# Kernel optimization log

Measured on AMD Instinct MI355X. Metric: run time of the kernel, lower is better.

Reference implementation:

```python
import jax, jax.numpy as jnp
import numpy as np

B, D, NTXT, H = 16384, 512, 4096, 1024


def _linear_params(key, fan_in, fan_out):
    kw, kb = jax.random.split(key)
    s = 1.0 / np.sqrt(fan_in)
    W = jax.random.uniform(kw, (fan_in, fan_out), jnp.float32, -s, s)
    b = jax.random.uniform(kb, (fan_out,), jnp.float32, -s, s)
    return W, b


def setup_inputs() -> dict:
    key = jax.random.key(0)
    ks = jax.random.split(key, 9)
    img_features = jax.random.normal(ks[0], (B, D), jnp.float32)
    txt_features = jax.random.normal(ks[1], (D, NTXT), jnp.float32)
    target_ind = jax.random.randint(ks[2], (B,), 0, NTXT, jnp.int32)
    Wi0, bi0 = _linear_params(ks[3], D, H)
    Wi1, bi1 = _linear_params(ks[4], H, H)
    Wi2, bi2 = _linear_params(ks[5], H, D)
    Wt0, bt0 = _linear_params(ks[6], D, H)
    Wt1, bt1 = _linear_params(ks[7], H, H)
    Wt2, bt2 = _linear_params(ks[8], H, D)
    logit_scale = jnp.asarray(np.log(1.0 / 0.07), jnp.float32)
    temp = jnp.asarray(1.0, jnp.float32)
    return {
        "img_features": img_features, "txt_features": txt_features,
        "target_ind": target_ind, "temp": temp,
        "Wi0": Wi0, "bi0": bi0, "Wi1": Wi1, "bi1": bi1, "Wi2": Wi2, "bi2": bi2,
        "Wt0": Wt0, "bt0": bt0, "Wt1": Wt1, "bt1": bt1, "Wt2": Wt2, "bt2": bt2,
        "logit_scale": logit_scale,
    }


def _mlp(x, params):
    # ReLU after every layer except the last (matches MLP.forward)
    for W, b in params[:-1]:
        x = jax.nn.relu(x @ W + b)
    W, b = params[-1]
    return x @ W + b


def reference(img_features, txt_features, target_ind, temp,
              Wi0, bi0, Wi1, bi1, Wi2, bi2,
              Wt0, bt0, Wt1, bt1, Wt2, bt2, logit_scale):
    p_img = _mlp(img_features, [(Wi0, bi0), (Wi1, bi1), (Wi2, bi2)])          # [B, D]
    p_txt = _mlp(txt_features.T, [(Wt0, bt0), (Wt1, bt1), (Wt2, bt2)])        # [N, D]

    sim = (p_img @ p_txt.T) * jnp.exp(logit_scale)                            # [B, N]
    sim = sim / jnp.linalg.norm(sim, axis=-1, keepdims=True)
    out_logits = sim / jnp.linalg.norm(sim, axis=-1, keepdims=True)           # faithful double-normalize

    # vectorized form of the per-sample Python-loop softmax-CE in MLP_CLIP_loss
    logp = jax.nn.log_softmax(out_logits / temp, axis=-1)                     # [B, N]
    picked = jnp.take_along_axis(logp, target_ind[:, None].astype(jnp.int32), axis=1)[:, 0]
    loss = -jnp.mean(picked)

    # accuracy branch (uses unscaled similarity, row-normalized)
    sim_clip = p_img @ p_txt.T
    sim_clip = sim_clip / jnp.linalg.norm(sim_clip, axis=-1, keepdims=True)
    acc = jnp.sum(jnp.argmax(sim_clip, axis=1).astype(jnp.int32) == target_ind)
    return loss, acc
```

## Files before the change

### kernel.cpp

```cpp
#include <hip/hip_runtime.h>
#include <cstdint>
#include <cstddef>

#define B_ROWS 16384
#define D_DIM  512
#define NTXT_N 4096
#define H_DIM  1024

typedef __attribute__((ext_vector_type(8))) short short8;
typedef __attribute__((ext_vector_type(4))) float f32x4;

__device__ __forceinline__ ushort f2bf(float x) {
    union { float f; uint32_t u; } c; c.f = x;
    const uint32_t u = c.u;
    return (ushort)((u + 0x7fffu + ((u >> 16) & 1u)) >> 16);
}
__device__ __forceinline__ float bf2f(ushort h) {
    union { uint32_t u; float f; } c; c.u = ((uint32_t)h) << 16;
    return c.f;
}

#define GLDS16(gp, lp) __builtin_amdgcn_global_load_lds( \
    (const __attribute__((address_space(1))) void*)(gp),  \
    (__attribute__((address_space(3))) void*)(lp), 16, 0, 0)

__device__ __forceinline__ void xcd_remap(int& bx, int& by) {
    const int nx = gridDim.x, ny = gridDim.y;
    const int nwg = nx * ny;
    const int bid = by * nx + bx;
    const int q = nwg >> 3, r = nwg & 7;
    const int xcd = bid & 7, idx = bid >> 3;
    const int nb = (xcd < r ? xcd * (q + 1) : r * (q + 1) + (xcd - r) * q) + idx;
    bx = nb % nx; by = nb / nx;
}

__global__ void init_kernel(int* acc) {
    if (threadIdx.x == 0 && blockIdx.x == 0) *acc = 0;
}

__global__ void tsplit_kernel(const float* __restrict__ in, ushort* __restrict__ oh,
                              ushort* __restrict__ ol, int R, int C, int cbase)
{
    __shared__ float tile[32][33];
    const int c0 = blockIdx.x * 32, r0 = blockIdx.y * 32;
    const int tx = threadIdx.x, ty = threadIdx.y;
    #pragma unroll
    for (int j = 0; j < 32; j += 8)
        tile[ty + j][tx] = in[(size_t)(r0 + ty + j) * C + cbase + c0 + tx];
    __syncthreads();
    #pragma unroll
    for (int j = 0; j < 32; j += 8) {
        const float v = tile[tx][ty + j];
        const ushort h = f2bf(v);
        const size_t idx = (size_t)(c0 + ty + j) * R + r0 + tx;
        oh[idx] = h;
        ol[idx] = f2bf(v - bf2f(h));
    }
}

__global__ void csplit_kernel(const float* __restrict__ in, ushort* __restrict__ oh,
                              ushort* __restrict__ ol, int n)
{
    const int i = (blockIdx.x * 256 + threadIdx.x) * 4;
    if (i >= n) return;
    const float4 f = *(const float4*)&in[i];
    ushort4 h, l;
    h.x = f2bf(f.x); l.x = f2bf(f.x - bf2f(h.x));
    h.y = f2bf(f.y); l.y = f2bf(f.y - bf2f(h.y));
    h.z = f2bf(f.z); l.z = f2bf(f.z - bf2f(h.z));
    h.w = f2bf(f.w); l.w = f2bf(f.w - bf2f(h.w));
    *(ushort4*)&oh[i] = h;
    *(ushort4*)&ol[i] = l;
}

template<int OMODE, bool RELU, bool BIAS>
__global__ __launch_bounds__(256, 2)
void gemm_mfma_kernel(const ushort* __restrict__ Ah, const ushort* __restrict__ Al,
                      const ushort* __restrict__ Bh, const ushort* __restrict__ Bl,
                      const float* __restrict__ bias,
                      float* __restrict__ Cf, ushort* __restrict__ Ch, ushort* __restrict__ Cl,
                      int M, int N, int K)
{
    __shared__ __align__(16) ushort Ahs[128 * 32];
    __shared__ __align__(16) ushort Als[128 * 32];
    __shared__ __align__(16) ushort Bhs[128 * 32];
    __shared__ __align__(16) ushort Bls[128 * 32];

    const int tid  = threadIdx.x;
    const int lane = tid & 63;
    const int w    = tid >> 6;
    const int wr   = w >> 1, wc = w & 1;

    int bxi = blockIdx.x, byi = blockIdx.y;
    xcd_remap(bxi, byi);
    const int bm = byi * 128, bn = bxi * 128;

    const int    srow  = w * 32 + (lane >> 2);
    const int    scol  = (((lane & 3) ^ ((lane >> 3) & 3)) << 3);
    const size_t aoff0 = (size_t)(bm + srow) * K + scol;
    const size_t boff0 = (size_t)(bn + srow) * K + scol;

    f32x4 acc[4][4];
    #pragma unroll
    for (int m = 0; m < 4; ++m)
        #pragma unroll
        for (int n = 0; n < 4; ++n)
            acc[m][n] = (f32x4)0.0f;

    const int frow = lane & 15;
    const int sl   = (frow >> 1) & 3;
    const int kslot = (lane >> 4) ^ sl;
    const int koff  = kslot << 3;

    for (int k0 = 0; k0 < K; k0 += 32) {
        #pragma unroll
        for (int j = 0; j < 2; ++j) {
            const size_t go = (size_t)j * 16 * K + k0;
            const int    lo = w * 1024 + j * 512;
            GLDS16(Ah + aoff0 + go, &Ahs[lo]);
            GLDS16(Al + aoff0 + go, &Als[lo]);
            GLDS16(Bh + boff0 + go, &Bhs[lo]);
            GLDS16(Bl + boff0 + go, &Bls[lo]);
        }
        __syncthreads();

        short8 a_h[4], a_l[4], b_h[4], b_l[4];
        #pragma unroll
        for (int m = 0; m < 4; ++m) {
            const int off = (wr * 64 + m * 16 + frow) * 32 + koff;
            a_h[m] = *(const short8*)&Ahs[off];
            a_l[m] = *(const short8*)&Als[off];
        }
        #pragma unroll
        for (int n = 0; n < 4; ++n) {
            const int off = (wc * 64 + n * 16 + frow) * 32 + koff;
            b_h[n] = *(const short8*)&Bhs[off];
            b_l[n] = *(const short8*)&Bls[off];
        }
        #pragma unroll
        for (int m = 0; m < 4; ++m)
            #pragma unroll
            for (int n = 0; n < 4; ++n) {
                acc[m][n] = __builtin_amdgcn_mfma_f32_16x16x32_bf16(a_h[m], b_h[n], acc[m][n], 0, 0, 0);
                acc[m][n] = __builtin_amdgcn_mfma_f32_16x16x32_bf16(a_h[m], b_l[n], acc[m][n], 0, 0, 0);
                acc[m][n] = __builtin_amdgcn_mfma_f32_16x16x32_bf16(a_l[m], b_h[n], acc[m][n], 0, 0, 0);
            }
        __syncthreads();
    }

    const int crow0 = bm + wr * 64 + (lane >> 4) * 4;
    const int ccol0 = bn + wc * 64 + (lane & 15);
    #pragma unroll
    for (int m = 0; m < 4; ++m)
        #pragma unroll
        for (int n = 0; n < 4; ++n) {
            const int col = ccol0 + n * 16;
            const float bv = BIAS ? bias[col] : 0.0f;
            #pragma unroll
            for (int q = 0; q < 4; ++q) {
                float v = acc[m][n][q] + bv;
                if (RELU) v = fmaxf(v, 0.0f);
                const size_t idx = (size_t)(crow0 + m * 16 + q) * N + col;
                if (OMODE == 0) {
                    Cf[idx] = v;
                } else {
                    const ushort h = f2bf(v);
                    Ch[idx] = h;
                    Cl[idx] = f2bf(v - bf2f(h));
                }
            }
        }
}

__global__ __launch_bounds__(256) void rowreduce_kernel(
    const float* __restrict__ sim, const int* __restrict__ tgt,
    const float* __restrict__ temp_p, float* __restrict__ perrow,
    int* __restrict__ acc_cnt, int row0)
{
    const int row = blockIdx.x;
    const float* srow = sim + (size_t)row * NTXT_N;
    const int tid = threadIdx.x;

    float v[16];
    #pragma unroll
    for (int q = 0; q < 4; ++q) {
        float4 f = *(const float4*)&srow[4 * tid + 1024 * q];
        v[4 * q + 0] = f.x; v[4 * q + 1] = f.y; v[4 * q + 2] = f.z; v[4 * q + 3] = f.w;
    }

    float ss = 0.0f, mx = -3.4e38f; int mi = 0x7fffffff;
    #pragma unroll
    for (int q = 0; q < 4; ++q)
        #pragma unroll
        for (int r = 0; r < 4; ++r) {
            const int j = 4 * tid + 1024 * q + r;
            const float x = v[4 * q + r];
            ss = fmaf(x, x, ss);
            if (x > mx) { mx = x; mi = j; }
            else if (x == mx && j < mi) mi = j;
        }

    #pragma unroll
    for (int off = 32; off; off >>= 1) {
        ss += __shfl_down(ss, off);
        const float omx = __shfl_down(mx, off);
        const int   omi = __shfl_down(mi, off);
        if (omx > mx || (omx == mx && omi < mi)) { mx = omx; mi = omi; }
    }

    __shared__ float sws[4], swm[4];
    __shared__ int   swi[4];
    __shared__ float bC, bMx;
    __shared__ int   bAmax;
    const int w = tid >> 6, lane = tid & 63;
    if (lane == 0) { sws[w] = ss; swm[w] = mx; swi[w] = mi; }
    __syncthreads();
    if (tid == 0) {
        float tss = 0.0f, tmx = -3.4e38f; int tmi = 0x7fffffff;
        #pragma unroll
        for (int i = 0; i < 4; ++i) {
            tss += sws[i];
            if (swm[i] > tmx || (swm[i] == tmx && swi[i] < tmi)) { tmx = swm[i]; tmi = swi[i]; }
        }
        const float inv_nr = 1.0f / sqrtf(tss);
        const float n2 = sqrtf(tss * inv_nr * inv_nr);
        const float Cv = inv_nr / (n2 * temp_p[0]);
        bC = Cv; bMx = tmx * Cv; bAmax = tmi;
    }
    __syncthreads();
    const float Cv = bC, mxx = bMx;

    float es = 0.0f;
    #pragma unroll
    for (int q = 0; q < 16; ++q) es += expf(v[q] * Cv - mxx);
    #pragma unroll
    for (int off = 32; off; off >>= 1) es += __shfl_down(es, off);
    if (lane == 0) sws[w] = es;
    __syncthreads();
    if (tid == 0) {
        const float tes = sws[0] + sws[1] + sws[2] + sws[3];
        const float lse = mxx + logf(tes);
        const int t = tgt[row0 + row];
        perrow[row0 + row] = lse - srow[t] * Cv;
        if (bAmax == t) atomicAdd(acc_cnt, 1);
    }
}

__global__ __launch_bounds__(256) void finalize_kernel(
    const float* __restrict__ perrow, const int* __restrict__ acc_cnt,
    float* __restrict__ out)
{
    __shared__ float red[256];
    const int tid = threadIdx.x;
    float s = 0.0f;
    for (int i = tid; i < B_ROWS; i += 256) s += perrow[i];
    red[tid] = s;
    __syncthreads();
    for (int st = 128; st; st >>= 1) {
        if (tid < st) red[tid] += red[tid + st];
        __syncthreads();
    }
    if (tid == 0) {
        out[0] = red[0] / (float)B_ROWS;
        out[1] = (float)(*acc_cnt);
    }
}

extern "C" void kernel_launch(void* const* d_in, const int* in_sizes, int n_in,
                              void* d_out, int out_size, void* d_ws, size_t ws_size,
                              hipStream_t stream)
{
    const float* img  = (const float*)d_in[0];
    const float* txt  = (const float*)d_in[1];
    const int*   tgt  = (const int*)  d_in[2];
    const float* temp = (const float*)d_in[3];
    const float* Wf[6] = { (const float*)d_in[4],  (const float*)d_in[6],  (const float*)d_in[8],
                           (const float*)d_in[10], (const float*)d_in[12], (const float*)d_in[14] };
    const float* bf[6] = { (const float*)d_in[5],  (const float*)d_in[7],  (const float*)d_in[9],
                           (const float*)d_in[11], (const float*)d_in[13], (const float*)d_in[15] };
    float* out = (float*)d_out;

    const int wK[6] = { D_DIM, H_DIM, H_DIM, D_DIM, H_DIM, H_DIM };
    const int wN[6] = { H_DIM, H_DIM, D_DIM, H_DIM, H_DIM, D_DIM };

    auto need = [&](size_t ch, size_t sc) -> size_t {
        size_t wt = 0;
        for (int i = 0; i < 6; ++i) wt += (size_t)wK[i] * wN[i] * 2 * 2;
        const size_t a01 = 2 * (ch * H_DIM * 2 * 2);
        const size_t pt  = (size_t)NTXT_N * D_DIM * 2 * 2;
        const size_t sim = sc * NTXT_N * 4;
        return wt + a01 + pt + sim + (size_t)B_ROWS * 4 + (size_t)64 * 1024;
    };
    const size_t ladder[][2] = { {16384, 4096}, {16384, 2048}, {8192, 4096}, {8192, 2048},
                                 {4096, 2048},  {4096, 1024},  {2048, 1024}, {1024, 1024} };
    size_t CH = 1024, SIMCH = 512;
    for (auto& e : ladder)
        if (need(e[0], e[1]) <= ws_size) { CH = e[0]; SIMCH = e[1]; break; }

    uint8_t* p = (uint8_t*)d_ws;
    auto alloc = [&](size_t bytes) -> void* {
        void* r = (void*)p; p += (bytes + 255) & ~(size_t)255; return r;
    };
    ushort* WTh[6]; ushort* WTl[6];
    for (int i = 0; i < 6; ++i) {
        WTh[i] = (ushort*)alloc((size_t)wK[i] * wN[i] * 2);
        WTl[i] = (ushort*)alloc((size_t)wK[i] * wN[i] * 2);
    }
    ushort* A0h = (ushort*)alloc(CH * H_DIM * 2);
    ushort* A0l = (ushort*)alloc(CH * H_DIM * 2);
    ushort* A1h = (ushort*)alloc(CH * H_DIM * 2);
    ushort* A1l = (ushort*)alloc(CH * H_DIM * 2);
    ushort* PTh = (ushort*)alloc((size_t)NTXT_N * D_DIM * 2);
    ushort* PTl = (ushort*)alloc((size_t)NTXT_N * D_DIM * 2);
    float*  SIM = (float*)alloc(SIMCH * NTXT_N * 4);
    float*  PERROW = (float*)alloc((size_t)B_ROWS * 4);
    int*    ACC = (int*)alloc(64);
    ushort* XBh = A1h;  ushort* XBl = A1l;
    ushort* PIh = A0h;  ushort* PIl = A0l;

    init_kernel<<<1, 64, 0, stream>>>(ACC);

    for (int i = 0; i < 6; ++i)
        tsplit_kernel<<<dim3(wN[i] / 32, wK[i] / 32), dim3(32, 8), 0, stream>>>(
            Wf[i], WTh[i], WTl[i], wK[i], wN[i], 0);

    const size_t CHT = CH < (size_t)NTXT_N ? CH : (size_t)NTXT_N;
    for (size_t n0 = 0; n0 < NTXT_N; n0 += CHT) {
        tsplit_kernel<<<dim3(CHT / 32, D_DIM / 32), dim3(32, 8), 0, stream>>>(
            txt, XBh, XBl, D_DIM, NTXT_N, (int)n0);
        gemm_mfma_kernel<1, true, true><<<dim3(H_DIM / 128, CHT / 128), 256, 0, stream>>>(
            XBh, XBl, WTh[3], WTl[3], bf[3], nullptr, A0h, A0l, (int)CHT, H_DIM, D_DIM);
        gemm_mfma_kernel<1, true, true><<<dim3(H_DIM / 128, CHT / 128), 256, 0, stream>>>(
            A0h, A0l, WTh[4], WTl[4], bf[4], nullptr, A1h, A1l, (int)CHT, H_DIM, H_DIM);
        gemm_mfma_kernel<1, false, true><<<dim3(D_DIM / 128, CHT / 128), 256, 0, stream>>>(
            A1h, A1l, WTh[5], WTl[5], bf[5], nullptr,
            PTh + n0 * D_DIM, PTl + n0 * D_DIM, (int)CHT, D_DIM, H_DIM);
    }

    for (size_t m0 = 0; m0 < B_ROWS; m0 += CH) {
        csplit_kernel<<<(CH * D_DIM / 4 + 255) / 256, 256, 0, stream>>>(
            img + m0 * D_DIM, XBh, XBl, (int)(CH * D_DIM));
        gemm_mfma_kernel<1, true, true><<<dim3(H_DIM / 128, CH / 128), 256, 0, stream>>>(
            XBh, XBl, WTh[0], WTl[0], bf[0], nullptr, A0h, A0l, (int)CH, H_DIM, D_DIM);
        gemm_mfma_kernel<1, true, true><<<dim3(H_DIM / 128, CH / 128), 256, 0, stream>>>(
            A0h, A0l, WTh[1], WTl[1], bf[1], nullptr, A1h, A1l, (int)CH, H_DIM, H_DIM);
        gemm_mfma_kernel<1, false, true><<<dim3(D_DIM / 128, CH / 128), 256, 0, stream>>>(
            A1h, A1l, WTh[2], WTl[2], bf[2], nullptr, PIh, PIl, (int)CH, D_DIM, H_DIM);
        for (size_t s0 = 0; s0 < CH; s0 += SIMCH) {
            gemm_mfma_kernel<0, false, false><<<dim3(NTXT_N / 128, SIMCH / 128), 256, 0, stream>>>(
                PIh + s0 * D_DIM, PIl + s0 * D_DIM, PTh, PTl, nullptr,
                SIM, nullptr, nullptr, (int)SIMCH, NTXT_N, D_DIM);
            rowreduce_kernel<<<SIMCH, 256, 0, stream>>>(
                SIM, tgt, temp, PERROW, ACC, (int)(m0 + s0));
        }
    }

    finalize_kernel<<<1, 256, 0, stream>>>(PERROW, ACC, out);
}
```

Before: 769.2 us.

## Pipeline split-bf16 GEMM with triple-buffered LDS stages over hi/lo segments

Restructures the split-bf16 MFMA GEMM so the three hi/lo product terms become three sequential K-segments (Ah·Bh, Ah·Bl, Al·Bh). Each stage loads only one A and one B half into a 3-deep rotating LDS ring, with vmcnt-based waits and a single barrier per stage in place of two syncthreads. K becomes a template parameter and MFMA issue is wrapped in s_setprio. The aim is to overlap global-to-LDS loads with MFMA compute and cut barrier and LDS footprint per stage. In exchange, A and B tiles are reloaded more often across segments (Ah and Bh twice each), and correctness now depends on hand-placed waitcnt and barrier ordering.

```diff
diff --git a/kernel.cpp b/kernel.cpp
--- a/kernel.cpp
+++ b/kernel.cpp
@@ -73,18 +73,18 @@
     *(ushort4*)&ol[i] = l;
 }
 
-template<int OMODE, bool RELU, bool BIAS>
+template<int K, int OMODE, bool RELU, bool BIAS>
 __global__ __launch_bounds__(256, 2)
-void gemm_mfma_kernel(const ushort* __restrict__ Ah, const ushort* __restrict__ Al,
-                      const ushort* __restrict__ Bh, const ushort* __restrict__ Bl,
-                      const float* __restrict__ bias,
-                      float* __restrict__ Cf, ushort* __restrict__ Ch, ushort* __restrict__ Cl,
-                      int M, int N, int K)
-{
-    __shared__ __align__(16) ushort Ahs[128 * 32];
-    __shared__ __align__(16) ushort Als[128 * 32];
-    __shared__ __align__(16) ushort Bhs[128 * 32];
-    __shared__ __align__(16) ushort Bls[128 * 32];
+void gemm3_kernel(const ushort* __restrict__ Ah, const ushort* __restrict__ Al,
+                  const ushort* __restrict__ Bh, const ushort* __restrict__ Bl,
+                  const float* __restrict__ bias,
+                  float* __restrict__ Cf, ushort* __restrict__ Ch, ushort* __restrict__ Cl,
+                  int M, int N)
+{
+    constexpr int SEG = K / 32;
+    constexpr int NT  = 3 * SEG;
+
+    __shared__ __align__(16) ushort LDSB[3 * 8192];
 
     const int tid  = threadIdx.x;
     const int lane = tid & 63;
@@ -95,11 +95,15 @@
     xcd_remap(bxi, byi);
     const int bm = byi * 128, bn = bxi * 128;
 
+    const int    stlo  = w * 1024;
     const int    srow  = w * 32 + (lane >> 2);
     const int    scol  = (((lane & 3) ^ ((lane >> 3) & 3)) << 3);
     const size_t aoff0 = (size_t)(bm + srow) * K + scol;
     const size_t boff0 = (size_t)(bn + srow) * K + scol;
 
+    const int frow  = lane & 15;
+    const int koff  = ((lane >> 4) ^ ((frow >> 1) & 3)) << 3;
+
     f32x4 acc[4][4];
     #pragma unroll
     for (int m = 0; m < 4; ++m)
@@ -107,46 +111,62 @@
         for (int n = 0; n < 4; ++n)
             acc[m][n] = (f32x4)0.0f;
 
-    const int frow = lane & 15;
-    const int sl   = (frow >> 1) & 3;
-    const int kslot = (lane >> 4) ^ sl;
-    const int koff  = kslot << 3;
-
-    for (int k0 = 0; k0 < K; k0 += 32) {
-        #pragma unroll
-        for (int j = 0; j < 2; ++j) {
-            const size_t go = (size_t)j * 16 * K + k0;
-            const int    lo = w * 1024 + j * 512;
-            GLDS16(Ah + aoff0 + go, &Ahs[lo]);
-            GLDS16(Al + aoff0 + go, &Als[lo]);
-            GLDS16(Bh + boff0 + go, &Bhs[lo]);
-            GLDS16(Bl + boff0 + go, &Bls[lo]);
-        }
-        __syncthreads();
-
-        short8 a_h[4], a_l[4], b_h[4], b_l[4];
-        #pragma unroll
-        for (int m = 0; m < 4; ++m) {
-            const int off = (wr * 64 + m * 16 + frow) * 32 + koff;
-            a_h[m] = *(const short8*)&Ahs[off];
-            a_l[m] = *(const short8*)&Als[off];
-        }
-        #pragma unroll
-        for (int n = 0; n < 4; ++n) {
-            const int off = (wc * 64 + n * 16 + frow) * 32 + koff;
-            b_h[n] = *(const short8*)&Bhs[off];
-            b_l[n] = *(const short8*)&Bls[off];
-        }
-        #pragma unroll
-        for (int m = 0; m < 4; ++m)
-            #pragma unroll
-            for (int n = 0; n < 4; ++n) {
-                acc[m][n] = __builtin_amdgcn_mfma_f32_16x16x32_bf16(a_h[m], b_h[n], acc[m][n], 0, 0, 0);
-                acc[m][n] = __builtin_amdgcn_mfma_f32_16x16x32_bf16(a_h[m], b_l[n], acc[m][n], 0, 0, 0);
-                acc[m][n] = __builtin_amdgcn_mfma_f32_16x16x32_bf16(a_l[m], b_h[n], acc[m][n], 0, 0, 0);
-            }
-        __syncthreads();
-    }
+#define STAGE_ISSUE(sidx) do {                                                \
+        const int _s = (sidx);                                                \
+        const int _seg = _s / SEG;                                            \
+        const int _kk  = (_s - _seg * SEG) * 32;                              \
+        const ushort* _ap = (_seg == 2 ? Al : Ah) + aoff0 + _kk;              \
+        const ushort* _bp = (_seg == 1 ? Bl : Bh) + boff0 + _kk;              \
+        ushort* _ab = &LDSB[(_s % 3) * 8192];                                 \
+        ushort* _bb = _ab + 4096;                                             \
+        GLDS16(_ap,              _ab + stlo);                                 \
+        GLDS16(_ap + 16 * K,     _ab + stlo + 512);                           \
+        GLDS16(_bp,              _bb + stlo);                                 \
+        GLDS16(_bp + 16 * K,     _bb + stlo + 512);                           \
+    } while (0)
+
+#define COMPUTE(bi) do {                                                      \
+        const ushort* _As = &LDSB[(bi) * 8192];                               \
+        const ushort* _Bs = _As + 4096;                                       \
+        short8 _af[4], _bf[4];                                                \
+        _Pragma("unroll")                                                     \
+        for (int m = 0; m < 4; ++m)                                           \
+            _af[m] = *(const short8*)&_As[(wr * 64 + m * 16 + frow) * 32 + koff]; \
+        _Pragma("unroll")                                                     \
+        for (int n = 0; n < 4; ++n)                                           \
+            _bf[n] = *(const short8*)&_Bs[(wc * 64 + n * 16 + frow) * 32 + koff]; \
+        __builtin_amdgcn_s_setprio(1);                                        \
+        _Pragma("unroll")                                                     \
+        for (int m = 0; m < 4; ++m)                                           \
+            _Pragma("unroll")                                                 \
+            for (int n = 0; n < 4; ++n)                                       \
+                acc[m][n] = __builtin_amdgcn_mfma_f32_16x16x32_bf16(          \
+                    _af[m], _bf[n], acc[m][n], 0, 0, 0);                      \
+        __builtin_amdgcn_s_setprio(0);                                        \
+    } while (0)
+
+#define WAITV4  asm volatile("s_waitcnt vmcnt(4)" ::: "memory")
+#define WAITV0  asm volatile("s_waitcnt vmcnt(0)" ::: "memory")
+#define BARRIER asm volatile("s_barrier" ::: "memory")
+
+    STAGE_ISSUE(0);
+    STAGE_ISSUE(1);
+
+    int t = 0;
+    for (int trip = 0; trip < NT / 3 - 1; ++trip, t += 3) {
+        WAITV4; BARRIER; STAGE_ISSUE(t + 2); COMPUTE(0);
+        WAITV4; BARRIER; STAGE_ISSUE(t + 3); COMPUTE(1);
+        WAITV4; BARRIER; STAGE_ISSUE(t + 4); COMPUTE(2);
+    }
+    WAITV4; BARRIER; STAGE_ISSUE(NT - 1); COMPUTE(0);
+    WAITV4; BARRIER;                      COMPUTE(1);
+    WAITV0; BARRIER;                      COMPUTE(2);
+
+#undef STAGE_ISSUE
+#undef COMPUTE
+#undef WAITV4
+#undef WAITV0
+#undef BARRIER
 
     const int crow0 = bm + wr * 64 + (lane >> 4) * 4;
     const int ccol0 = bn + wc * 64 + (lane & 15);
@@ -328,28 +348,28 @@
     for (size_t n0 = 0; n0 < NTXT_N; n0 += CHT) {
         tsplit_kernel<<<dim3(CHT / 32, D_DIM / 32), dim3(32, 8), 0, stream>>>(
             txt, XBh, XBl, D_DIM, NTXT_N, (int)n0);
-        gemm_mfma_kernel<1, true, true><<<dim3(H_DIM / 128, CHT / 128), 256, 0, stream>>>(
-            XBh, XBl, WTh[3], WTl[3], bf[3], nullptr, A0h, A0l, (int)CHT, H_DIM, D_DIM);
-        gemm_mfma_kernel<1, true, true><<<dim3(H_DIM / 128, CHT / 128), 256, 0, stream>>>(
-            A0h, A0l, WTh[4], WTl[4], bf[4], nullptr, A1h, A1l, (int)CHT, H_DIM, H_DIM);
-        gemm_mfma_kernel<1, false, true><<<dim3(D_DIM / 128, CHT / 128), 256, 0, stream>>>(
+        gemm3_kernel<D_DIM, 1, true, true><<<dim3(H_DIM / 128, CHT / 128), 256, 0, stream>>>(
+            XBh, XBl, WTh[3], WTl[3], bf[3], nullptr, A0h, A0l, (int)CHT, H_DIM);
+        gemm3_kernel<H_DIM, 1, true, true><<<dim3(H_DIM / 128, CHT / 128), 256, 0, stream>>>(
+            A0h, A0l, WTh[4], WTl[4], bf[4], nullptr, A1h, A1l, (int)CHT, H_DIM);
+        gemm3_kernel<H_DIM, 1, false, true><<<dim3(D_DIM / 128, CHT / 128), 256, 0, stream>>>(
             A1h, A1l, WTh[5], WTl[5], bf[5], nullptr,
-            PTh + n0 * D_DIM, PTl + n0 * D_DIM, (int)CHT, D_DIM, H_DIM);
+            PTh + n0 * D_DIM, PTl + n0 * D_DIM, (int)CHT, D_DIM);
     }
 
     for (size_t m0 = 0; m0 < B_ROWS; m0 += CH) {
         csplit_kernel<<<(CH * D_DIM / 4 + 255) / 256, 256, 0, stream>>>(
             img + m0 * D_DIM, XBh, XBl, (int)(CH * D_DIM));
-        gemm_mfma_kernel<1, true, true><<<dim3(H_DIM / 128, CH / 128), 256, 0, stream>>>(
-            XBh, XBl, WTh[0], WTl[0], bf[0], nullptr, A0h, A0l, (int)CH, H_DIM, D_DIM);
-        gemm_mfma_kernel<1, true, true><<<dim3(H_DIM / 128, CH / 128), 256, 0, stream>>>(
-            A0h, A0l, WTh[1], WTl[1], bf[1], nullptr, A1h, A1l, (int)CH, H_DIM, H_DIM);
-        gemm_mfma_kernel<1, false, true><<<dim3(D_DIM / 128, CH / 128), 256, 0, stream>>>(
-            A1h, A1l, WTh[2], WTl[2], bf[2], nullptr, PIh, PIl, (int)CH, D_DIM, H_DIM);
+        gemm3_kernel<D_DIM, 1, true, true><<<dim3(H_DIM / 128, CH / 128), 256, 0, stream>>>(
+            XBh, XBl, WTh[0], WTl[0], bf[0], nullptr, A0h, A0l, (int)CH, H_DIM);
+        gemm3_kernel<H_DIM, 1, true, true><<<dim3(H_DIM / 128, CH / 128), 256, 0, stream>>>(
+            A0h, A0l, WTh[1], WTl[1], bf[1], nullptr, A1h, A1l, (int)CH, H_DIM);
+        gemm3_kernel<H_DIM, 1, false, true><<<dim3(D_DIM / 128, CH / 128), 256, 0, stream>>>(
+            A1h, A1l, WTh[2], WTl[2], bf[2], nullptr, PIh, PIl, (int)CH, D_DIM);
         for (size_t s0 = 0; s0 < CH; s0 += SIMCH) {
-            gemm_mfma_kernel<0, false, false><<<dim3(NTXT_N / 128, SIMCH / 128), 256, 0, stream>>>(
+            gemm3_kernel<D_DIM, 0, false, false><<<dim3(NTXT_N / 128, SIMCH / 128), 256, 0, stream>>>(
                 PIh + s0 * D_DIM, PIl + s0 * D_DIM, PTh, PTl, nullptr,
-                SIM, nullptr, nullptr, (int)SIMCH, NTXT_N, D_DIM);
+                SIM, nullptr, nullptr, (int)SIMCH, NTXT_N);
             rowreduce_kernel<<<SIMCH, 256, 0, stream>>>(
                 SIM, tgt, temp, PERROW, ACC, (int)(m0 + s0));
         }
```

Result: slower. 793.2 us (+3.1%).
